# Kernel optimization log

Hardware: AMD Instinct MI355X
Metric: run time of the kernel (lower is better)

The kernel has to match this reference:

```python
import jax, jax.numpy as jnp
import numpy as np

H = 16          # num_attention_heads
HD = 64         # attention_head_size
D = H * HD
SCALE = HD ** -0.5
SP_HEADS = np.array([0, 2, 4, 6, 8, 10, 12, 14])   # sparsemax heads
SM_HEADS = np.array([1, 3, 5, 7, 9, 11, 13, 15])   # softmax heads


def sparsemax(z):
    # z: [..., K]; sparsemax along last dim (Martins & Astudillo 2016)
    K = z.shape[-1]
    zs = -jnp.sort(-z, axis=-1)                      # descending sort
    k = jnp.arange(1, K + 1, dtype=z.dtype)
    cs = jnp.cumsum(zs, axis=-1)
    support = (1 + k * zs) > cs
    ksel = jnp.sum(support, axis=-1, keepdims=True)  # support size >= 1
    tau = (jnp.take_along_axis(cs, ksel - 1, axis=-1) - 1) / ksel.astype(z.dtype)
    return jnp.maximum(z - tau, 0)


def setup_inputs() -> dict:
    key = jax.random.key(0)
    ks = jax.random.split(key, 4)
    B, S = 4, 1024
    return {
        "hidden_states": jax.random.normal(ks[0], (B, S, D), dtype=jnp.float32),
        "Wq": jax.random.normal(ks[1], (D, D), dtype=jnp.float32) * 0.02,
        "bq": jnp.zeros((D,), dtype=jnp.float32),
        "Wk": jax.random.normal(ks[2], (D, D), dtype=jnp.float32) * 0.02,
        "bk": jnp.zeros((D,), dtype=jnp.float32),
        "Wv": jax.random.normal(ks[3], (D, D), dtype=jnp.float32) * 0.02,
        "bv": jnp.zeros((D,), dtype=jnp.float32),
        "attention_mask": jnp.zeros((B, 1, 1, S), dtype=jnp.float32),
    }


def reference(hidden_states, Wq, bq, Wk, bk, Wv, bv, attention_mask):
    B, S, _ = hidden_states.shape

    def proj(W, b):
        # [B,S,D] -> [B,H,S,HD]
        return (hidden_states @ W + b).reshape(B, S, H, HD).transpose(0, 2, 1, 3)

    q, k, v = proj(Wq, bq), proj(Wk, bk), proj(Wv, bv)
    scores = jnp.einsum('bhqd,bhkd->bhqk', q, k) * SCALE
    scores = scores + attention_mask
    scores = jnp.maximum(scores, -10000.0)           # clamp(min=-10000)
    weights = jnp.zeros_like(scores)
    weights = weights.at[:, SP_HEADS].set(sparsemax(scores[:, SP_HEADS]))
    weights = weights.at[:, SM_HEADS].set(jax.nn.softmax(scores[:, SM_HEADS], axis=-1))
    # dropout_p = 0 in eval mode
    attn_out = jnp.einsum('bhqk,bhkd->bhqd', weights, v)
    attn_out = attn_out.transpose(0, 2, 1, 3).reshape(B, S, D)
    return attn_out
```

## Files before the change

### kernel.cpp

```cpp
#include <hip/hip_runtime.h>
#include <hip/hip_bf16.h>
#include <stdint.h>

#define NH 16
#define HD 64
#define DM 1024
#define NB 4
#define SEQ 1024
#define NTOK (NB*SEQ)
#define SCALE 0.125f

typedef __bf16 bf16_t;
typedef __bf16 bf16x8 __attribute__((ext_vector_type(8)));
typedef __bf16 bf16x4 __attribute__((ext_vector_type(4)));
typedef float f32x4 __attribute__((ext_vector_type(4)));

typedef __attribute__((address_space(3))) unsigned char lds_byte;
typedef __attribute__((address_space(1))) const unsigned char gbl_byte;

__device__ __forceinline__ void glds16(const void* g, void* l){
  __builtin_amdgcn_global_load_lds((gbl_byte*)g, (lds_byte*)l, 16, 0, 0);
}

__global__ void cvt_hs_kernel(const float* __restrict__ in, bf16_t* __restrict__ out, int n4){
  int i = blockIdx.x*256 + threadIdx.x;
  if (i >= n4) return;
  f32x4 v = ((const f32x4*)in)[i];
  bf16x4 o;
  o[0]=(bf16_t)v[0]; o[1]=(bf16_t)v[1]; o[2]=(bf16_t)v[2]; o[3]=(bf16_t)v[3];
  ((bf16x4*)out)[i] = o;
}

__global__ void cvt_wt_kernel(const float* __restrict__ Wq, const float* __restrict__ Wk,
                              const float* __restrict__ Wv, bf16_t* __restrict__ outbase){
  __shared__ float tile[32][33];
  const float* W = blockIdx.z==0 ? Wq : (blockIdx.z==1 ? Wk : Wv);
  bf16_t* Wt = outbase + (size_t)blockIdx.z * DM * DM;
  int k0 = blockIdx.x*32, n0 = blockIdx.y*32;
  #pragma unroll
  for (int i=0;i<4;i++){
    int r = threadIdx.y + i*8;
    tile[r][threadIdx.x] = W[(size_t)(k0+r)*DM + n0 + threadIdx.x];
  }
  __syncthreads();
  #pragma unroll
  for (int i=0;i<4;i++){
    int r = threadIdx.y + i*8;
    Wt[(size_t)(n0+r)*DM + k0 + threadIdx.x] = (bf16_t)tile[threadIdx.x][r];
  }
}

__global__ __launch_bounds__(256)
void qkv_gemm_kernel(const bf16_t* __restrict__ Ag, const bf16_t* __restrict__ Wtb,
                     const float* __restrict__ bq, const float* __restrict__ bk, const float* __restrict__ bv,
                     bf16_t* __restrict__ Qb, bf16_t* __restrict__ Kb, bf16_t* __restrict__ Vb)
{
  __shared__ __align__(16) bf16_t smem[2*128*64];
  bf16_t* Asm = smem;
  bf16_t* Bsm = smem + 128*64;
  bf16_t* Csm = smem;
  const int z = blockIdx.z;
  const bf16_t* Btg = Wtb + (size_t)z*DM*DM;
  const float* bias = (z==0)?bq:((z==1)?bk:bv);
  bf16_t* dst = (z==0)?Qb:((z==1)?Kb:Vb);
  const int m0 = blockIdx.x*128, n0 = blockIdx.y*128;
  const int tid = threadIdx.x, lane = tid&63, w = tid>>6;
  const int wr = w>>1, wc = w&1;
  const int lr = lane&15, hk = (lane>>4)<<3;

  f32x4 acc[4][4];
  #pragma unroll
  for (int a=0;a<4;a++)
    #pragma unroll
    for (int c=0;c<4;c++)
      acc[a][c] = (f32x4){0.f,0.f,0.f,0.f};

  for (int k0=0; k0<DM; k0+=64){
    #pragma unroll
    for (int i=0;i<4;i++){
      int cb = (i<<8) + (tid & 448);
      int flat = cb + lane;
      int row = flat>>3, kc = (flat&7)<<3;
      glds16(&Ag [(size_t)(m0+row)*DM + k0 + kc], &Asm[cb<<3]);
      glds16(&Btg[(size_t)(n0+row)*DM + k0 + kc], &Bsm[cb<<3]);
    }
    __syncthreads();
    #pragma unroll
    for (int kk=0;kk<2;kk++){
      bf16x8 af[4], bfv[4];
      #pragma unroll
      for (int mf=0;mf<4;mf++)
        af[mf] = *(const bf16x8*)&Asm[((wr*64 + mf*16 + lr)<<6) + (kk<<5) + hk];
      #pragma unroll
      for (int nf=0;nf<4;nf++)
        bfv[nf] = *(const bf16x8*)&Bsm[((wc*64 + nf*16 + lr)<<6) + (kk<<5) + hk];
      #pragma unroll
      for (int mf=0;mf<4;mf++)
        #pragma unroll
        for (int nf=0;nf<4;nf++)
          acc[mf][nf] = __builtin_amdgcn_mfma_f32_16x16x32_bf16(af[mf], bfv[nf], acc[mf][nf], 0, 0, 0);
    }
    __syncthreads();
  }

  const int q4 = (lane>>4)<<2;
  #pragma unroll
  for (int mf=0;mf<4;mf++){
    #pragma unroll
    for (int nf=0;nf<4;nf++){
      int col = wc*64 + nf*16 + lr;
      float bsv = bias[n0 + col];
      #pragma unroll
      for (int j=0;j<4;j++)
        Csm[(wr*64 + mf*16 + q4 + j)*128 + col] = (bf16_t)(acc[mf][nf][j] + bsv);
    }
  }
  __syncthreads();
  {
    int row = tid>>1, half = tid&1;
    int gm = m0 + row, bb = gm>>10, sq = gm&1023;
    int hh = (n0 + half*64)>>6;
    const bf16x8* src = (const bf16x8*)&Csm[row*128 + half*64];
    bf16x8* d = (bf16x8*)&dst[(((size_t)bb*NH + hh)*SEQ + sq)*HD];
    #pragma unroll
    for (int c=0;c<8;c++) d[c] = src[c];
  }
}

__global__ __launch_bounds__(256)
void v_tr_kernel(const bf16_t* __restrict__ Vb, bf16_t* __restrict__ Vt){
  __shared__ __align__(16) bf16_t T[64*64];
  const int bh = blockIdx.y, sq0 = blockIdx.x*64;
  const int t = threadIdx.x;
  const bf16_t* src = Vb + ((size_t)bh*SEQ + sq0)*HD;
  #pragma unroll
  for (int i=0;i<2;i++){
    int flat = i*256 + t;
    int r = flat>>3, ch = flat&7;
    bf16x8 v = *(const bf16x8*)&src[r*HD + ch*8];
    *(bf16x8*)((char*)T + r*128 + ((ch ^ (r&7))*16)) = v;
  }
  __syncthreads();
  const int hd = t>>2, part = t&3;
  bf16_t tmp[16];
  #pragma unroll
  for (int s=0;s<16;s++){
    int sq = part*16 + s;
    tmp[s] = *(const bf16_t*)((char*)T + sq*128 + (((hd>>3) ^ (sq&7))*16) + (hd&7)*2);
  }
  bf16_t* d = Vt + ((size_t)bh*HD + hd)*SEQ + sq0 + part*16;
  *(bf16x8*)&d[0] = *(const bf16x8*)&tmp[0];
  *(bf16x8*)&d[8] = *(const bf16x8*)&tmp[8];
}

__device__ __forceinline__ void red4sum(float v[4]){
  #pragma unroll
  for (int m=32;m>=1;m>>=1){
    float t0=__shfl_xor(v[0],m,64), t1=__shfl_xor(v[1],m,64);
    float t2=__shfl_xor(v[2],m,64), t3=__shfl_xor(v[3],m,64);
    v[0]+=t0; v[1]+=t1; v[2]+=t2; v[3]+=t3;
  }
}
__device__ __forceinline__ void red4max(float v[4]){
  #pragma unroll
  for (int m=32;m>=1;m>>=1){
    float t0=__shfl_xor(v[0],m,64), t1=__shfl_xor(v[1],m,64);
    float t2=__shfl_xor(v[2],m,64), t3=__shfl_xor(v[3],m,64);
    v[0]=fmaxf(v[0],t0); v[1]=fmaxf(v[1],t1); v[2]=fmaxf(v[2],t2); v[3]=fmaxf(v[3],t3);
  }
}

__global__ __launch_bounds__(512)
void attn_mfma2_kernel(const bf16_t* __restrict__ Qg, const bf16_t* __restrict__ Kg,
                       const bf16_t* __restrict__ Vt, const float* __restrict__ maskg,
                       float* __restrict__ outg)
{
  __shared__ __align__(16) bf16_t Sb[32*1024];
  char* Sbb = (char*)Sb;

  const int flat = blockIdx.x;
  const int xcd = flat & 7, jj = flat >> 3;
  const int bh = ((jj>>5)<<3) | xcd;
  const int row0 = (jj&31)*32;
  const int b = bh>>4, h = bh&15;
  const int tid = threadIdx.x, lane = tid&63, w = tid>>6;
  const int ln = lane&15, hi4 = lane>>4;
  const size_t hoff = (size_t)bh*SEQ*HD;
  const int kbase = w*128;

  bf16x8 qf[2][2];
  #pragma unroll
  for (int mt=0; mt<2; ++mt)
    #pragma unroll
    for (int kt=0; kt<2; ++kt)
      qf[mt][kt] = *(const bf16x8*)&Qg[hoff + (size_t)(row0 + mt*16 + ln)*HD + kt*32 + hi4*8];

  #pragma unroll
  for (int nt=0; nt<8; ++nt){
    const int krow = kbase + nt*16;
    bf16x8 kf0 = *(const bf16x8*)&Kg[hoff + (size_t)(krow+ln)*HD +  0 + hi4*8];
    bf16x8 kf1 = *(const bf16x8*)&Kg[hoff + (size_t)(krow+ln)*HD + 32 + hi4*8];
    f32x4 mv = *(const f32x4*)&maskg[(size_t)b*SEQ + krow + hi4*4];
    #pragma unroll
    for (int mt=0; mt<2; ++mt){
      f32x4 acc = (f32x4){0.f,0.f,0.f,0.f};
      acc = __builtin_amdgcn_mfma_f32_16x16x32_bf16(kf0, qf[mt][0], acc, 0,0,0);
      acc = __builtin_amdgcn_mfma_f32_16x16x32_bf16(kf1, qf[mt][1], acc, 0,0,0);
      bf16x4 pk;
      #pragma unroll
      for (int j=0;j<4;++j)
        pk[j] = (bf16_t)fmaxf(fmaf(acc[j], SCALE, mv[j]), -10000.f);
      const int q = mt*16 + ln;
      const int g = (krow + hi4*4) >> 3;
      const int gp = g ^ ln;
      *(bf16x4*)(Sbb + q*2048 + gp*16 + (hi4&1)*8) = pk;
    }
  }
  __syncthreads();

  float z[4][16];
  const int qr = w*4;
  #pragma unroll
  for (int r=0;r<4;++r){
    const int q = qr + r;
    #pragma unroll
    for (int i=0;i<4;++i){
      const int gp = (i*32 + (lane>>1)) ^ (q&15);
      bf16x4 v4 = *(const bf16x4*)(Sbb + q*2048 + gp*16 + (lane&1)*8);
      z[r][i*4+0]=(float)v4[0]; z[r][i*4+1]=(float)v4[1];
      z[r][i*4+2]=(float)v4[2]; z[r][i*4+3]=(float)v4[3];
    }
  }
  __syncthreads();

  float mx[4];
  #pragma unroll
  for (int r=0;r<4;++r){
    float m = z[r][0];
    #pragma unroll
    for (int i=1;i<16;++i) m = fmaxf(m, z[r][i]);
    mx[r] = m;
  }
  red4max(mx);

  if ((h&1)==0){
    float lo[4], hi_[4];
    #pragma unroll
    for (int r=0;r<4;++r){ lo[r]=mx[r]-1.0f; hi_[r]=mx[r]; }
    for (int it=0; it<8; ++it){
      float mid[4], g4[4];
      #pragma unroll
      for (int r=0;r<4;++r){
        mid[r] = 0.5f*(lo[r]+hi_[r]);
        float g = 0.f;
        #pragma unroll
        for (int i=0;i<16;++i) g += fmaxf(z[r][i]-mid[r], 0.f);
        g4[r] = g;
      }
      red4sum(g4);
      #pragma unroll
      for (int r=0;r<4;++r){
        if (g4[r] >= 1.0f) lo[r] = mid[r]; else hi_[r] = mid[r];
      }
    }
    float tau[4];
    #pragma unroll
    for (int r=0;r<4;++r) tau[r] = lo[r];
    for (int it=0; it<3; ++it){
      float cnt[4], sm[4];
      #pragma unroll
      for (int r=0;r<4;++r){
        float c=0.f, s=0.f;
        #pragma unroll
        for (int i=0;i<16;++i){
          bool in = z[r][i] > tau[r];
          c += in ? 1.0f : 0.0f;
          s += in ? z[r][i] : 0.0f;
        }
        cnt[r]=c; sm[r]=s;
      }
      red4sum(cnt); red4sum(sm);
      #pragma unroll
      for (int r=0;r<4;++r) tau[r] = (sm[r]-1.0f)/cnt[r];
    }
    #pragma unroll
    for (int r=0;r<4;++r)
      #pragma unroll
      for (int i=0;i<16;++i) z[r][i] = fmaxf(z[r][i]-tau[r], 0.f);
  } else {
    float sm[4];
    #pragma unroll
    for (int r=0;r<4;++r){
      float s = 0.f;
      #pragma unroll
      for (int i=0;i<16;++i){ z[r][i] = __expf(z[r][i]-mx[r]); s += z[r][i]; }
      sm[r] = s;
    }
    red4sum(sm);
    #pragma unroll
    for (int r=0;r<4;++r){
      float inv = 1.0f/sm[r];
      #pragma unroll
      for (int i=0;i<16;++i) z[r][i] *= inv;
    }
  }

  #pragma unroll
  for (int r=0;r<4;++r){
    const int q = qr + r;
    #pragma unroll
    for (int i=0;i<4;++i){
      bf16x4 pk;
      pk[0]=(bf16_t)z[r][i*4+0]; pk[1]=(bf16_t)z[r][i*4+1];
      pk[2]=(bf16_t)z[r][i*4+2]; pk[3]=(bf16_t)z[r][i*4+3];
      const int gp = (i*32 + (lane>>1)) ^ (q&15);
      *(bf16x4*)(Sbb + q*2048 + gp*16 + (lane&1)*8) = pk;
    }
  }
  __syncthreads();

  const int mt = w>>2, hd0 = (w&3)*16;
  const bf16_t* vrow = Vt + (size_t)bh*HD*SEQ + (size_t)(hd0+ln)*SEQ;
  const char* wrow = Sbb + (mt*16+ln)*2048;
  f32x4 o0 = (f32x4){0.f,0.f,0.f,0.f}, o1 = (f32x4){0.f,0.f,0.f,0.f};
  #pragma unroll
  for (int kt=0; kt<32; kt+=2){
    bf16x8 wa0 = *(const bf16x8*)(wrow + ((((kt+0)*4+hi4) ^ ln)<<4));
    bf16x8 vb0 = *(const bf16x8*)&vrow[(kt+0)*32 + hi4*8];
    o0 = __builtin_amdgcn_mfma_f32_16x16x32_bf16(wa0, vb0, o0, 0,0,0);
    bf16x8 wa1 = *(const bf16x8*)(wrow + ((((kt+1)*4+hi4) ^ ln)<<4));
    bf16x8 vb1 = *(const bf16x8*)&vrow[(kt+1)*32 + hi4*8];
    o1 = __builtin_amdgcn_mfma_f32_16x16x32_bf16(wa1, vb1, o1, 0,0,0);
  }
  o0 += o1;

  __syncthreads();
  float* Ob = (float*)Sbb;
  #pragma unroll
  for (int j=0;j<4;++j)
    Ob[(mt*16 + hi4*4 + j)*64 + hd0 + ln] = o0[j];
  __syncthreads();
  {
    int rr = tid>>4, c4 = (tid&15)<<2;
    *(f32x4*)&outg[(size_t)(b*SEQ + row0 + rr)*DM + h*64 + c4] = *(const f32x4*)&Ob[rr*64 + c4];
  }
}

extern "C" void kernel_launch(void* const* d_in, const int* in_sizes, int n_in,
                              void* d_out, int out_size, void* d_ws, size_t ws_size,
                              hipStream_t stream)
{
  const float* hs   = (const float*)d_in[0];
  const float* Wq   = (const float*)d_in[1];
  const float* bq   = (const float*)d_in[2];
  const float* Wk   = (const float*)d_in[3];
  const float* bk   = (const float*)d_in[4];
  const float* Wv   = (const float*)d_in[5];
  const float* bv   = (const float*)d_in[6];
  const float* mask = (const float*)d_in[7];
  float* out = (float*)d_out;

  char* ws = (char*)d_ws;
  bf16_t* hsb = (bf16_t*)ws;
  bf16_t* Wt  = (bf16_t*)(ws + (size_t)( 8u<<20));
  bf16_t* Qb  = (bf16_t*)(ws + (size_t)(14u<<20));
  bf16_t* Kb  = (bf16_t*)(ws + (size_t)(22u<<20));
  bf16_t* Vb  = (bf16_t*)(ws + (size_t)(30u<<20));
  bf16_t* Vt  = hsb;

  cvt_hs_kernel<<<(NTOK*DM/4 + 255)/256, 256, 0, stream>>>(hs, hsb, NTOK*DM/4);
  cvt_wt_kernel<<<dim3(32,32,3), dim3(32,8), 0, stream>>>(Wq, Wk, Wv, Wt);
  qkv_gemm_kernel<<<dim3(32,8,3), 256, 0, stream>>>(hsb, Wt, bq, bk, bv, Qb, Kb, Vb);
  v_tr_kernel<<<dim3(16,64), 256, 0, stream>>>(Vb, Vt);
  attn_mfma2_kernel<<<2048, 512, 0, stream>>>(Qb, Kb, Vt, mask, out);
}
```

Baseline: 368.3 us.

## Halve attention query tile to 16 rows and split PV over key halves

The attention kernel now handles 16 query rows per block instead of 32, doubling the grid to 4096 blocks and cutting LDS per block from 64KB to 40KB, which can allow more blocks per CU. The PV stage splits the 1024-key reduction across two wave groups, each summing 512 keys, and adds the partial results through an LDS buffer. One barrier between reading scores and normalizing is removed, and the sparsemax count and sum reductions are merged into one shuffle pass. In exchange, each block re-reads the full K and V for half as many queries, so global and L2 traffic doubles.

Result: faster. 315.2 us (-14.4%).

```diff
diff --git a/kernel.cpp b/kernel.cpp
--- a/kernel.cpp
+++ b/kernel.cpp
@@ -153,6 +153,20 @@
   *(bf16x8*)&d[8] = *(const bf16x8*)&tmp[8];
 }
 
+__device__ __forceinline__ void red2sum(float v[2]){
+  #pragma unroll
+  for (int m=32;m>=1;m>>=1){
+    float t0=__shfl_xor(v[0],m,64), t1=__shfl_xor(v[1],m,64);
+    v[0]+=t0; v[1]+=t1;
+  }
+}
+__device__ __forceinline__ void red2max(float v[2]){
+  #pragma unroll
+  for (int m=32;m>=1;m>>=1){
+    float t0=__shfl_xor(v[0],m,64), t1=__shfl_xor(v[1],m,64);
+    v[0]=fmaxf(v[0],t0); v[1]=fmaxf(v[1],t1);
+  }
+}
 __device__ __forceinline__ void red4sum(float v[4]){
   #pragma unroll
   for (int m=32;m>=1;m>>=1){
@@ -161,39 +175,28 @@
     v[0]+=t0; v[1]+=t1; v[2]+=t2; v[3]+=t3;
   }
 }
-__device__ __forceinline__ void red4max(float v[4]){
-  #pragma unroll
-  for (int m=32;m>=1;m>>=1){
-    float t0=__shfl_xor(v[0],m,64), t1=__shfl_xor(v[1],m,64);
-    float t2=__shfl_xor(v[2],m,64), t3=__shfl_xor(v[3],m,64);
-    v[0]=fmaxf(v[0],t0); v[1]=fmaxf(v[1],t1); v[2]=fmaxf(v[2],t2); v[3]=fmaxf(v[3],t3);
-  }
-}
 
 __global__ __launch_bounds__(512)
-void attn_mfma2_kernel(const bf16_t* __restrict__ Qg, const bf16_t* __restrict__ Kg,
+void attn_mfma3_kernel(const bf16_t* __restrict__ Qg, const bf16_t* __restrict__ Kg,
                        const bf16_t* __restrict__ Vt, const float* __restrict__ maskg,
                        float* __restrict__ outg)
 {
-  __shared__ __align__(16) bf16_t Sb[32*1024];
+  __shared__ __align__(16) bf16_t Sb[20*1024];
   char* Sbb = (char*)Sb;
+  float* Pacc = (float*)(Sbb + 32768);
 
   const int flat = blockIdx.x;
   const int xcd = flat & 7, jj = flat >> 3;
-  const int bh = ((jj>>5)<<3) | xcd;
-  const int row0 = (jj&31)*32;
+  const int bh = ((jj>>6)<<3) | xcd;
+  const int row0 = (jj&63)*16;
   const int b = bh>>4, h = bh&15;
   const int tid = threadIdx.x, lane = tid&63, w = tid>>6;
   const int ln = lane&15, hi4 = lane>>4;
   const size_t hoff = (size_t)bh*SEQ*HD;
   const int kbase = w*128;
 
-  bf16x8 qf[2][2];
-  #pragma unroll
-  for (int mt=0; mt<2; ++mt)
-    #pragma unroll
-    for (int kt=0; kt<2; ++kt)
-      qf[mt][kt] = *(const bf16x8*)&Qg[hoff + (size_t)(row0 + mt*16 + ln)*HD + kt*32 + hi4*8];
+  bf16x8 qf0 = *(const bf16x8*)&Qg[hoff + (size_t)(row0 + ln)*HD +  0 + hi4*8];
+  bf16x8 qf1 = *(const bf16x8*)&Qg[hoff + (size_t)(row0 + ln)*HD + 32 + hi4*8];
 
   #pragma unroll
   for (int nt=0; nt<8; ++nt){
@@ -201,75 +204,68 @@
     bf16x8 kf0 = *(const bf16x8*)&Kg[hoff + (size_t)(krow+ln)*HD +  0 + hi4*8];
     bf16x8 kf1 = *(const bf16x8*)&Kg[hoff + (size_t)(krow+ln)*HD + 32 + hi4*8];
     f32x4 mv = *(const f32x4*)&maskg[(size_t)b*SEQ + krow + hi4*4];
-    #pragma unroll
-    for (int mt=0; mt<2; ++mt){
-      f32x4 acc = (f32x4){0.f,0.f,0.f,0.f};
-      acc = __builtin_amdgcn_mfma_f32_16x16x32_bf16(kf0, qf[mt][0], acc, 0,0,0);
-      acc = __builtin_amdgcn_mfma_f32_16x16x32_bf16(kf1, qf[mt][1], acc, 0,0,0);
-      bf16x4 pk;
-      #pragma unroll
-      for (int j=0;j<4;++j)
-        pk[j] = (bf16_t)fmaxf(fmaf(acc[j], SCALE, mv[j]), -10000.f);
-      const int q = mt*16 + ln;
-      const int g = (krow + hi4*4) >> 3;
-      const int gp = g ^ ln;
-      *(bf16x4*)(Sbb + q*2048 + gp*16 + (hi4&1)*8) = pk;
-    }
-  }
-  __syncthreads();
-
-  float z[4][16];
-  const int qr = w*4;
-  #pragma unroll
-  for (int r=0;r<4;++r){
-    const int q = qr + r;
+    f32x4 acc = (f32x4){0.f,0.f,0.f,0.f};
+    acc = __builtin_amdgcn_mfma_f32_16x16x32_bf16(kf0, qf0, acc, 0,0,0);
+    acc = __builtin_amdgcn_mfma_f32_16x16x32_bf16(kf1, qf1, acc, 0,0,0);
+    bf16x4 pk;
+    #pragma unroll
+    for (int j=0;j<4;++j)
+      pk[j] = (bf16_t)fmaxf(fmaf(acc[j], SCALE, mv[j]), -10000.f);
+    const int g = (krow + hi4*4) >> 3;
+    const int gp = g ^ ln;
+    *(bf16x4*)(Sbb + ln*2048 + gp*16 + (hi4&1)*8) = pk;
+  }
+  __syncthreads();
+
+  float z[2][16];
+  #pragma unroll
+  for (int r=0;r<2;++r){
+    const int q = w*2 + r;
     #pragma unroll
     for (int i=0;i<4;++i){
-      const int gp = (i*32 + (lane>>1)) ^ (q&15);
+      const int gp = (i*32 + (lane>>1)) ^ q;
       bf16x4 v4 = *(const bf16x4*)(Sbb + q*2048 + gp*16 + (lane&1)*8);
       z[r][i*4+0]=(float)v4[0]; z[r][i*4+1]=(float)v4[1];
       z[r][i*4+2]=(float)v4[2]; z[r][i*4+3]=(float)v4[3];
     }
   }
-  __syncthreads();
-
-  float mx[4];
-  #pragma unroll
-  for (int r=0;r<4;++r){
+
+  float mx[2];
+  #pragma unroll
+  for (int r=0;r<2;++r){
     float m = z[r][0];
     #pragma unroll
     for (int i=1;i<16;++i) m = fmaxf(m, z[r][i]);
     mx[r] = m;
   }
-  red4max(mx);
+  red2max(mx);
 
   if ((h&1)==0){
-    float lo[4], hi_[4];
-    #pragma unroll
-    for (int r=0;r<4;++r){ lo[r]=mx[r]-1.0f; hi_[r]=mx[r]; }
+    float lo[2], hi_[2];
+    #pragma unroll
+    for (int r=0;r<2;++r){ lo[r]=mx[r]-1.0f; hi_[r]=mx[r]; }
     for (int it=0; it<8; ++it){
-      float mid[4], g4[4];
-      #pragma unroll
-      for (int r=0;r<4;++r){
-        mid[r] = 0.5f*(lo[r]+hi_[r]);
+      float g2[2];
+      #pragma unroll
+      for (int r=0;r<2;++r){
+        float mid = 0.5f*(lo[r]+hi_[r]);
         float g = 0.f;
         #pragma unroll
-        for (int i=0;i<16;++i) g += fmaxf(z[r][i]-mid[r], 0.f);
-        g4[r] = g;
+        for (int i=0;i<16;++i) g += fmaxf(z[r][i]-mid, 0.f);
+        g2[r] = g;
       }
-      red4sum(g4);
-      #pragma unroll
-      for (int r=0;r<4;++r){
-        if (g4[r] >= 1.0f) lo[r] = mid[r]; else hi_[r] = mid[r];
+      red2sum(g2);
+      #pragma unroll
+      for (int r=0;r<2;++r){
+        float mid = 0.5f*(lo[r]+hi_[r]);
+        if (g2[r] >= 1.0f) lo[r] = mid; else hi_[r] = mid;
       }
     }
-    float tau[4];
-    #pragma unroll
-    for (int r=0;r<4;++r) tau[r] = lo[r];
+    float tau[2] = {lo[0], lo[1]};
     for (int it=0; it<3; ++it){
-      float cnt[4], sm[4];
-      #pragma unroll
-      for (int r=0;r<4;++r){
+      float cs[4];
+      #pragma unroll
+      for (int r=0;r<2;++r){
         float c=0.f, s=0.f;
         #pragma unroll
         for (int i=0;i<16;++i){
@@ -277,28 +273,28 @@
           c += in ? 1.0f : 0.0f;
           s += in ? z[r][i] : 0.0f;
         }
-        cnt[r]=c; sm[r]=s;
+        cs[r]=c; cs[2+r]=s;
       }
-      red4sum(cnt); red4sum(sm);
-      #pragma unroll
-      for (int r=0;r<4;++r) tau[r] = (sm[r]-1.0f)/cnt[r];
-    }
-    #pragma unroll
-    for (int r=0;r<4;++r)
+      red4sum(cs);
+      #pragma unroll
+      for (int r=0;r<2;++r) tau[r] = (cs[2+r]-1.0f)/cs[r];
+    }
+    #pragma unroll
+    for (int r=0;r<2;++r)
       #pragma unroll
       for (int i=0;i<16;++i) z[r][i] = fmaxf(z[r][i]-tau[r], 0.f);
   } else {
-    float sm[4];
-    #pragma unroll
-    for (int r=0;r<4;++r){
+    float sm[2];
+    #pragma unroll
+    for (int r=0;r<2;++r){
       float s = 0.f;
       #pragma unroll
       for (int i=0;i<16;++i){ z[r][i] = __expf(z[r][i]-mx[r]); s += z[r][i]; }
       sm[r] = s;
     }
-    red4sum(sm);
-    #pragma unroll
-    for (int r=0;r<4;++r){
+    red2sum(sm);
+    #pragma unroll
+    for (int r=0;r<2;++r){
       float inv = 1.0f/sm[r];
       #pragma unroll
       for (int i=0;i<16;++i) z[r][i] *= inv;
@@ -306,43 +302,44 @@
   }
 
   #pragma unroll
-  for (int r=0;r<4;++r){
-    const int q = qr + r;
+  for (int r=0;r<2;++r){
+    const int q = w*2 + r;
     #pragma unroll
     for (int i=0;i<4;++i){
       bf16x4 pk;
       pk[0]=(bf16_t)z[r][i*4+0]; pk[1]=(bf16_t)z[r][i*4+1];
       pk[2]=(bf16_t)z[r][i*4+2]; pk[3]=(bf16_t)z[r][i*4+3];
-      const int gp = (i*32 + (lane>>1)) ^ (q&15);
+      const int gp = (i*32 + (lane>>1)) ^ q;
       *(bf16x4*)(Sbb + q*2048 + gp*16 + (lane&1)*8) = pk;
     }
   }
   __syncthreads();
 
-  const int mt = w>>2, hd0 = (w&3)*16;
-  const bf16_t* vrow = Vt + (size_t)bh*HD*SEQ + (size_t)(hd0+ln)*SEQ;
-  const char* wrow = Sbb + (mt*16+ln)*2048;
+  const int kh = w>>2, nt = w&3;
+  const bf16_t* vrow = Vt + (size_t)bh*HD*SEQ + (size_t)(nt*16+ln)*SEQ + kh*512;
+  const char* wrow = Sbb + ln*2048;
   f32x4 o0 = (f32x4){0.f,0.f,0.f,0.f}, o1 = (f32x4){0.f,0.f,0.f,0.f};
   #pragma unroll
-  for (int kt=0; kt<32; kt+=2){
-    bf16x8 wa0 = *(const bf16x8*)(wrow + ((((kt+0)*4+hi4) ^ ln)<<4));
+  for (int kt=0; kt<16; kt+=2){
+    int g0 = kh*64 + (kt+0)*4 + hi4;
+    bf16x8 wa0 = *(const bf16x8*)(wrow + ((g0 ^ ln)<<4));
     bf16x8 vb0 = *(const bf16x8*)&vrow[(kt+0)*32 + hi4*8];
     o0 = __builtin_amdgcn_mfma_f32_16x16x32_bf16(wa0, vb0, o0, 0,0,0);
-    bf16x8 wa1 = *(const bf16x8*)(wrow + ((((kt+1)*4+hi4) ^ ln)<<4));
+    int g1 = kh*64 + (kt+1)*4 + hi4;
+    bf16x8 wa1 = *(const bf16x8*)(wrow + ((g1 ^ ln)<<4));
     bf16x8 vb1 = *(const bf16x8*)&vrow[(kt+1)*32 + hi4*8];
     o1 = __builtin_amdgcn_mfma_f32_16x16x32_bf16(wa1, vb1, o1, 0,0,0);
   }
   o0 += o1;
-
-  __syncthreads();
-  float* Ob = (float*)Sbb;
   #pragma unroll
   for (int j=0;j<4;++j)
-    Ob[(mt*16 + hi4*4 + j)*64 + hd0 + ln] = o0[j];
-  __syncthreads();
-  {
-    int rr = tid>>4, c4 = (tid&15)<<2;
-    *(f32x4*)&outg[(size_t)(b*SEQ + row0 + rr)*DM + h*64 + c4] = *(const f32x4*)&Ob[rr*64 + c4];
+    Pacc[(kh*16 + hi4*4 + j)*64 + nt*16 + ln] = o0[j];
+  __syncthreads();
+
+  if (tid < 256){
+    int q = tid>>4, c4 = (tid&15)<<2;
+    f32x4 s = *(const f32x4*)&Pacc[q*64 + c4] + *(const f32x4*)&Pacc[(16+q)*64 + c4];
+    *(f32x4*)&outg[(size_t)(b*SEQ + row0 + q)*DM + h*64 + c4] = s;
   }
 }
 
@@ -372,5 +369,5 @@
   cvt_wt_kernel<<<dim3(32,32,3), dim3(32,8), 0, stream>>>(Wq, Wk, Wv, Wt);
   qkv_gemm_kernel<<<dim3(32,8,3), 256, 0, stream>>>(hsb, Wt, bq, bk, bv, Qb, Kb, Vb);
   v_tr_kernel<<<dim3(16,64), 256, 0, stream>>>(Vb, Vt);
-  attn_mfma2_kernel<<<2048, 512, 0, stream>>>(Qb, Kb, Vt, mask, out);
-}
+  attn_mfma3_kernel<<<4096, 512, 0, stream>>>(Qb, Kb, Vt, mask, out);
+}
```
